# Kernel optimization log

Hardware: AMD Instinct MI355X
Metric: run time of the kernel (lower is better)

Reference implementation:

```python
import jax, jax.numpy as jnp
import numpy as np

B = 8          # graphs (FOVs)
NPG = 16384    # clusters per graph
N = B * NPG
K = 6          # knn k=5+1, loop=True
E = N * K
C0PG = 2048    # superclusters_0 per graph
C0 = B * C0PG
C1PG = 256     # superclusters_1 per graph
C1 = B * C1PG
L = 10         # 4 cluster-level + 3 SC0 + 3 SC1 PointTransformerConv layers
D = 64


def setup_inputs() -> dict:
    key = jax.random.key(0)
    ks = jax.random.split(key, 20)
    s = 0.05  # weight scale for stable attention logits
    x = jax.random.normal(ks[0], (N, D), jnp.float32)
    pos_c = jax.random.uniform(ks[1], (N, 2), jnp.float32)
    dst_c = jnp.repeat(jnp.arange(N, dtype=jnp.int32), K)
    src_c = jax.random.randint(ks[2], (E,), 0, N, jnp.int32)
    src_c = src_c.at[::K].set(jnp.arange(N, dtype=jnp.int32))  # self-loops
    batch = (jnp.arange(N, dtype=jnp.int32) // NPG)
    sc_id0 = (jnp.arange(N, dtype=jnp.int32) % C0PG)   # every SC0 id present per graph
    pos_sc0 = jax.random.uniform(ks[3], (C0, 2), jnp.float32)
    sc_id1 = (jnp.arange(C0, dtype=jnp.int32) % C1PG)
    pos_sc1 = jax.random.uniform(ks[4], (C1, 2), jnp.float32)
    return dict(
        x=x, pos_c=pos_c, src_c=src_c, dst_c=dst_c, batch=batch,
        sc_id0=sc_id0, pos_sc0=pos_sc0, sc_id1=sc_id1, pos_sc1=pos_sc1,
        Wlin=jax.random.normal(ks[5], (L, D, D)) * s,
        Wsrc=jax.random.normal(ks[6], (L, D, D)) * s,
        Wdst=jax.random.normal(ks[7], (L, D, D)) * s,
        pW1=jax.random.normal(ks[8], (L, 2, D)) * s,
        pB1=jnp.zeros((L, D), jnp.float32),
        pW2=jax.random.normal(ks[9], (L, D, D)) * s,
        pB2=jnp.zeros((L, D), jnp.float32),
        aW1=jax.random.normal(ks[10], (L, D, D)) * s,
        aB1=jnp.zeros((L, D), jnp.float32),
        aW2=jax.random.normal(ks[11], (L, D, D)) * s,
        aB2=jnp.zeros((L, D), jnp.float32),
        head_w=jax.random.normal(ks[12], (D, 2)) * s,
        head_b=jnp.zeros((2,), jnp.float32),
    )


def mlp2(x, W1, b1, W2, b2):
    # PyG MLP(plain_last=False): Linear->ReLU twice (eval mode, BN at init = identity)
    h = jax.nn.relu(x @ W1 + b1)
    return jax.nn.relu(h @ W2 + b2)


def ptconv(h, pos, src, dst, n, p, l):
    # PointTransformerConv: delta = pos_nn(pos_i - pos_j);
    # alpha = softmax_i(attn_nn(lin_dst(x)_i - lin_src(x)_j + delta));
    # out_i = max_j alpha * (lin(x)_j + delta)
    xv = h @ p['Wlin'][l]
    a_src = h @ p['Wsrc'][l]
    a_dst = h @ p['Wdst'][l]
    delta = mlp2(pos[dst] - pos[src], p['pW1'][l], p['pB1'][l], p['pW2'][l], p['pB2'][l])
    a = mlp2(a_dst[dst] - a_src[src] + delta, p['aW1'][l], p['aB1'][l], p['aW2'][l], p['aB2'][l])
    m = jax.ops.segment_max(a, dst, num_segments=n)
    e = jnp.exp(a - m[dst])
    ssum = jax.ops.segment_sum(e, dst, num_segments=n)
    alpha = e / ssum[dst]
    return jax.ops.segment_max(alpha * (xv[src] + delta), dst, num_segments=n)


def gen_cluster(ids, batch, nb):
    mx = jax.ops.segment_max(ids, batch, num_segments=nb)
    off = jnp.cumsum(jnp.concatenate([jnp.zeros((1,), ids.dtype), mx + 1]))
    return ids + off[batch].astype(ids.dtype)


def knn_edges(pos, b, npg, k):
    # knn_graph(k, loop=True) per graph: src=neighbor, dst=center
    p = pos.reshape(b, npg, 2)
    sq = jnp.sum(p * p, axis=-1)
    d2 = sq[:, :, None] + sq[:, None, :] - 2.0 * jnp.einsum('bnd,bmd->bnm', p, p)
    idx = jax.lax.top_k(-d2, k)[1]  # [b, npg, k], includes self (d=0)
    src = (idx + (jnp.arange(b) * npg)[:, None, None]).reshape(-1).astype(jnp.int32)
    dst = jnp.repeat(jnp.arange(b * npg, dtype=jnp.int32), k)
    return src, dst


def reference(x, pos_c, src_c, dst_c, batch, sc_id0, pos_sc0, sc_id1, pos_sc1,
              Wlin, Wsrc, Wdst, pW1, pB1, pW2, pB2, aW1, aB1, aW2, aB2,
              head_w, head_b):
    p = dict(Wlin=Wlin, Wsrc=Wsrc, Wdst=Wdst, pW1=pW1, pB1=pB1, pW2=pW2, pB2=pB2,
             aW1=aW1, aB1=aB1, aW2=aW2, aB2=aB2)
    h = x
    for l in range(4):  # cluster_encoder_0..3 on clusters graph
        h = ptconv(h, pos_c, src_c, dst_c, N, p, l)
    # pool clusters -> superclusters_0
    cl0 = gen_cluster(sc_id0, batch, B)
    h0 = jax.ops.segment_max(h, cl0, num_segments=C0)
    batch0 = jax.ops.segment_max(batch, cl0, num_segments=C0)
    src0, dst0 = knn_edges(pos_sc0, B, C0PG, K)
    for l in range(4, 7):
        h0 = ptconv(h0, pos_sc0, src0, dst0, C0, p, l)
    # pool SC0 -> superclusters_1
    cl1 = gen_cluster(sc_id1, batch0, B)
    h1 = jax.ops.segment_max(h0, cl1, num_segments=C1)
    batch1 = jax.ops.segment_max(batch0, cl1, num_segments=C1)
    src1, dst1 = knn_edges(pos_sc1, B, C1PG, K)
    for l in range(7, 10):
        h1 = ptconv(h1, pos_sc1, src1, dst1, C1, p, l)
    g = jax.ops.segment_max(h1, batch1, num_segments=B)  # global_max_pool
    return g @ head_w + head_b
```

## Files before the change

### kernel.cpp

```cpp
#include <hip/hip_runtime.h>
#include <cstdint>

namespace {
constexpr int BG   = 8;
constexpr int NPG  = 16384;
constexpr int NN   = BG * NPG;
constexpr int KK   = 6;
constexpr int C0PG = 2048;
constexpr int C0N  = BG * C0PG;
constexpr int C1PG = 256;
constexpr int C1N  = BG * C1PG;
constexpr int D    = 64;
constexpr int SEG0 = C0PG / 256;
constexpr int VS8  = 260;
constexpr int NMS  = 132;
}

__device__ __forceinline__ unsigned f2u_ord(float v) {
  unsigned u = __float_as_uint(v);
  return (u & 0x80000000u) ? ~u : (u | 0x80000000u);
}

__global__ void k_init_u32(unsigned* __restrict__ p, unsigned v, int n) {
  int i = blockIdx.x * blockDim.x + threadIdx.x;
  if (i < n) p[i] = v;
}

__global__ void k_seg_max_i32(const int* __restrict__ vals, const int* __restrict__ seg,
                              int* __restrict__ out, int n) {
  int i = blockIdx.x * blockDim.x + threadIdx.x;
  if (i < n) atomicMax(&out[seg[i]], vals[i]);
}

template <int NB>
__global__ __launch_bounds__(256) void k_seg_max_small(
    const int* __restrict__ vals, const int* __restrict__ seg,
    int* __restrict__ out, int n) {
  __shared__ int lmx[NB];
  int t = threadIdx.x;
  if (t < NB) lmx[t] = (int)0x80000000;
  __syncthreads();
  for (int i = blockIdx.x * 256 + t; i < n; i += gridDim.x * 256)
    atomicMax(&lmx[seg[i]], vals[i]);
  __syncthreads();
  if (t < NB) atomicMax(&out[t], lmx[t]);
}

__global__ void k_cumsum_off(const int* __restrict__ mx, int* __restrict__ off, int nb) {
  if (threadIdx.x == 0 && blockIdx.x == 0) {
    int a = 0; off[0] = 0;
    for (int b = 0; b < nb; ++b) { a += mx[b] + 1; off[b + 1] = a; }
  }
}

__global__ void k_gen_cl(const int* __restrict__ ids, const int* __restrict__ bt,
                         const int* __restrict__ off, int* __restrict__ cl, int n) {
  int i = blockIdx.x * blockDim.x + threadIdx.x;
  if (i < n) cl[i] = ids[i] + off[bt[i]];
}

__global__ void k_pool_f32(const float* __restrict__ h, const int* __restrict__ cl,
                           unsigned* __restrict__ outu, int total) {
  int i = blockIdx.x * blockDim.x + threadIdx.x;
  if (i < total) atomicMax(&outu[(size_t)cl[i >> 6] * D + (i & 63)], f2u_ord(h[i]));
}

__global__ void k_decode_f32(unsigned* __restrict__ p, int n) {
  int i = blockIdx.x * blockDim.x + threadIdx.x;
  if (i < n) { unsigned u = p[i]; p[i] = (u & 0x80000000u) ? (u ^ 0x80000000u) : ~u; }
}

__global__ __launch_bounds__(256) void k_knn(const float* __restrict__ pos, int npg,
                                             int* __restrict__ srcOut) {
  #pragma clang fp contract(off)
  __shared__ float px[2048], py[2048], sq[2048];
  int t = threadIdx.x;
  int nglob = blockIdx.x * 256 + t;
  int graph = nglob / npg;
  int base = graph * npg;
  for (int i = t; i < npg; i += 256) {
    float xx = pos[2 * (base + i)];
    float yy = pos[2 * (base + i) + 1];
    px[i] = xx; py[i] = yy;
    float a = xx * xx; float b = yy * yy;
    sq[i] = a + b;
  }
  __syncthreads();
  int i = nglob - base;
  float xi = px[i], yi = py[i], sqi = sq[i];
  float bd[KK]; int bi[KK];
  #pragma unroll
  for (int q = 0; q < KK; ++q) { bd[q] = 3.4e38f; bi[q] = 0; }
  for (int j = 0; j < npg; ++j) {
    float t1 = xi * px[j];
    float t2 = yi * py[j];
    float dot = t1 + t2;
    float d2 = (sqi + sq[j]) - 2.0f * dot;
    if (d2 < bd[KK - 1]) {
      bd[KK - 1] = d2; bi[KK - 1] = j;
      #pragma unroll
      for (int q = KK - 1; q > 0; --q) {
        if (bd[q] < bd[q - 1]) {
          float td = bd[q]; bd[q] = bd[q - 1]; bd[q - 1] = td;
          int ti = bi[q]; bi[q] = bi[q - 1]; bi[q - 1] = ti;
        }
      }
    }
  }
  #pragma unroll
  for (int q = 0; q < KK; ++q) srcOut[(size_t)nglob * KK + q] = base + bi[q];
}

__global__ __launch_bounds__(256) void k_knn_part(const float* __restrict__ pos, int npg,
                                                  int nseg,
                                                  float* __restrict__ outD,
                                                  int* __restrict__ outI) {
  #pragma clang fp contract(off)
  __shared__ float cx[256], cy[256], cs[256];
  int t = threadIdx.x;
  int qt = blockIdx.x / nseg;
  int s  = blockIdx.x % nseg;
  int qlo = qt * 256;
  int graph = qlo / npg;
  int base = graph * npg;
  int cbase = base + s * 256;
  {
    float xx = pos[2 * (cbase + t)];
    float yy = pos[2 * (cbase + t) + 1];
    cx[t] = xx; cy[t] = yy;
    float a = xx * xx; float b = yy * yy;
    cs[t] = a + b;
  }
  __syncthreads();
  int q = qlo + t;
  float xi = pos[2 * q], yi = pos[2 * q + 1];
  float qa = xi * xi; float qb = yi * yi;
  float sqi = qa + qb;
  float bd[KK]; int bi[KK];
  #pragma unroll
  for (int u = 0; u < KK; ++u) { bd[u] = 3.4e38f; bi[u] = 0; }
  for (int j = 0; j < 256; ++j) {
    float t1 = xi * cx[j];
    float t2 = yi * cy[j];
    float dot = t1 + t2;
    float d2 = (sqi + cs[j]) - 2.0f * dot;
    if (d2 < bd[KK - 1]) {
      bd[KK - 1] = d2; bi[KK - 1] = cbase + j;
      #pragma unroll
      for (int u = KK - 1; u > 0; --u) {
        if (bd[u] < bd[u - 1]) {
          float td = bd[u]; bd[u] = bd[u - 1]; bd[u - 1] = td;
          int ti = bi[u]; bi[u] = bi[u - 1]; bi[u - 1] = ti;
        }
      }
    }
  }
  size_t ob = (size_t)q * (nseg * KK) + (size_t)s * KK;
  #pragma unroll
  for (int u = 0; u < KK; ++u) { outD[ob + u] = bd[u]; outI[ob + u] = bi[u]; }
}

__global__ void k_knn_merge(const float* __restrict__ inD, const int* __restrict__ inI,
                            int nseg, int* __restrict__ srcOut, int nq) {
  int q = blockIdx.x * blockDim.x + threadIdx.x;
  if (q >= nq) return;
  float bd[KK]; int bi[KK];
  #pragma unroll
  for (int u = 0; u < KK; ++u) { bd[u] = 3.4e38f; bi[u] = 0x7fffffff; }
  size_t ib = (size_t)q * (nseg * KK);
  for (int e = 0; e < nseg * KK; ++e) {
    float d = inD[ib + e]; int ix = inI[ib + e];
    bool lt = (d < bd[KK - 1]) || (d == bd[KK - 1] && ix < bi[KK - 1]);
    if (lt) {
      bd[KK - 1] = d; bi[KK - 1] = ix;
      #pragma unroll
      for (int u = KK - 1; u > 0; --u) {
        bool sw = (bd[u] < bd[u - 1]) || (bd[u] == bd[u - 1] && bi[u] < bi[u - 1]);
        if (sw) {
          float td = bd[u]; bd[u] = bd[u - 1]; bd[u - 1] = td;
          int ti = bi[u]; bi[u] = bi[u - 1]; bi[u - 1] = ti;
        }
      }
    }
  }
  #pragma unroll
  for (int u = 0; u < KK; ++u) srcOut[(size_t)q * KK + u] = bi[u];
}

__global__ void __launch_bounds__(256)
__attribute__((amdgpu_waves_per_eu(4, 4)))
k_node_mm(const float* __restrict__ hin,
    const float* __restrict__ Wl, const float* __restrict__ Ws, const float* __restrict__ Wd,
    float* __restrict__ xv, float* __restrict__ as_, float* __restrict__ ad_) {
  __shared__ float wbuf[2048];
  __shared__ float vbuf[32 * NMS];
  int t = threadIdx.x;
  size_t nb = (size_t)blockIdx.x * 128;
  int ng = t >> 3, cb = t & 7, c0 = cb * 8;
  const float* Wm[3] = {Wl, Ws, Wd};
  float* Om[3] = {xv, as_, ad_};
  const float4* h4 = (const float4*)hin;
  float acc[3][32];
  #pragma unroll
  for (int m = 0; m < 3; ++m)
    #pragma unroll
    for (int i = 0; i < 32; ++i) acc[m][i] = 0.0f;
  for (int kh = 0; kh < 2; ++kh) {
    #pragma unroll
    for (int r = 0; r < 4; ++r) {
      int flat = r * 256 + t;
      int n = flat >> 3, kq = flat & 7;
      float4 hv = h4[(nb + n) * 16 + kh * 8 + kq];
      vbuf[(kq * 4 + 0) * NMS + n] = hv.x;
      vbuf[(kq * 4 + 1) * NMS + n] = hv.y;
      vbuf[(kq * 4 + 2) * NMS + n] = hv.z;
      vbuf[(kq * 4 + 3) * NMS + n] = hv.w;
    }
    #pragma unroll
    for (int m = 0; m < 3; ++m) {
      {
        const float4* w4 = (const float4*)Wm[m] + kh * 512;
        float4* wb = (float4*)wbuf;
        wb[t] = w4[t];
        wb[256 + t] = w4[256 + t];
      }
      __syncthreads();
      #pragma clang loop unroll_count(2)
      for (int kk = 0; kk < 32; ++kk) {
        float4 v4 = *(const float4*)&vbuf[kk * NMS + 4 * ng];
        float4 w0 = *(const float4*)&wbuf[kk * 64 + c0];
        float4 w1 = *(const float4*)&wbuf[kk * 64 + c0 + 4];
        float vv[4] = {v4.x, v4.y, v4.z, v4.w};
        float wv[8] = {w0.x, w0.y, w0.z, w0.w, w1.x, w1.y, w1.z, w1.w};
        #pragma unroll
        for (int ni = 0; ni < 4; ++ni)
          #pragma unroll
          for (int c = 0; c < 8; ++c)
            acc[m][ni * 8 + c] = fmaf(vv[ni], wv[c], acc[m][ni * 8 + c]);
      }
      __syncthreads();
    }
  }
  #pragma unroll
  for (int m = 0; m < 3; ++m) {
    float* O = Om[m];
    #pragma unroll
    for (int ni = 0; ni < 4; ++ni) {
      *(float4*)(O + (nb + 4 * ng + ni) * 64 + c0) =
          make_float4(acc[m][ni * 8 + 0], acc[m][ni * 8 + 1],
                      acc[m][ni * 8 + 2], acc[m][ni * 8 + 3]);
      *(float4*)(O + (nb + 4 * ng + ni) * 64 + c0 + 4) =
          make_float4(acc[m][ni * 8 + 4], acc[m][ni * 8 + 5],
                      acc[m][ni * 8 + 6], acc[m][ni * 8 + 7]);
    }
  }
}

__global__ void __launch_bounds__(256)
__attribute__((amdgpu_waves_per_eu(3, 3)))
k_edge_fused(
    const float* __restrict__ pos, const int* __restrict__ srcA,
    const float* __restrict__ as_, const float* __restrict__ ad_,
    const float* __restrict__ xv,
    const float* __restrict__ pW1, const float* __restrict__ pB1,
    const float* __restrict__ pW2, const float* __restrict__ pB2,
    const float* __restrict__ aW1, const float* __restrict__ aB1,
    const float* __restrict__ aW2, const float* __restrict__ aB2,
    float* __restrict__ hout) {
  __shared__ float wbuf[2048];
  __shared__ float vbuf[32 * VS8];
  __shared__ float sbuf[192];
  __shared__ float pdxs[192], pdys[192];
  __shared__ int   srcb[192];
  int t = threadIdx.x;
  int nb = blockIdx.x * 32;
  int ng = t >> 3;
  int cb = t & 7;
  int cl = 4 * cb;
  int ch = 32 + 4 * cb;
  int node = nb + ng;
  int ecol = 8 * ng;

  float4 wreg0 = ((const float4*)pW2)[t];
  float4 wreg1 = ((const float4*)pW2)[256 + t];
  int mycol = 8 * (t / 6) + (t % 6);
  if (t < 192) {
    int s = srcA[(size_t)nb * KK + t];
    srcb[t] = s;
    int dn = nb + t / KK;
    float2 pd = *(const float2*)(pos + 2 * (size_t)dn);
    float2 ps = *(const float2*)(pos + 2 * (size_t)s);
    pdxs[t] = pd.x - ps.x;
    pdys[t] = pd.y - ps.y;
    sbuf[t] = (t < 128) ? pW1[t] : pB1[t - 128];
  }
  __syncthreads();

  float d[48];
  {
    float4 b0 = *(const float4*)(pB2 + cl);
    float4 b1 = *(const float4*)(pB2 + ch);
    #pragma unroll
    for (int j = 0; j < 6; ++j) {
      d[j * 8 + 0] = b0.x; d[j * 8 + 1] = b0.y; d[j * 8 + 2] = b0.z; d[j * 8 + 3] = b0.w;
      d[j * 8 + 4] = b1.x; d[j * 8 + 5] = b1.y; d[j * 8 + 6] = b1.z; d[j * 8 + 7] = b1.w;
    }
  }
  #pragma unroll
  for (int h = 0; h < 2; ++h) {
    {
      float4* wb = (float4*)wbuf;
      wb[t] = wreg0;
      wb[256 + t] = wreg1;
    }
    {
      const float4* nxt = (h == 0) ? ((const float4*)pW2 + 512) : ((const float4*)aW1);
      wreg0 = nxt[t];
      wreg1 = nxt[256 + t];
    }
    if (t < 192) {
      float px = pdxs[t], py = pdys[t];
      #pragma clang loop unroll_count(4)
      for (int kk = 0; kk < 32; ++kk) {
        int k = h * 32 + kk;
        float p0 = px * sbuf[k];
        float p1 = py * sbuf[64 + k];
        float ph = fmaxf((p0 + p1) + sbuf[128 + k], 0.0f);
        vbuf[kk * VS8 + mycol] = ph;
      }
    }
    __syncthreads();
    #pragma clang loop unroll_count(2)
    for (int kk = 0; kk < 32; ++kk) {
      float4 va = *(const float4*)&vbuf[kk * VS8 + ecol];
      float4 vb = *(const float4*)&vbuf[kk * VS8 + ecol + 4];
      float4 w0 = *(const float4*)&wbuf[kk * 64 + cl];
      float4 w1 = *(const float4*)&wbuf[kk * 64 + ch];
      float vv[6] = {va.x, va.y, va.z, va.w, vb.x, vb.y};
      float wv[8] = {w0.x, w0.y, w0.z, w0.w, w1.x, w1.y, w1.z, w1.w};
      #pragma unroll
      for (int j = 0; j < 6; ++j)
        #pragma unroll
        for (int c = 0; c < 8; ++c)
          d[j * 8 + c] = fmaf(vv[j], wv[c], d[j * 8 + c]);
    }
    __syncthreads();
  }
  #pragma unroll
  for (int i = 0; i < 48; ++i) d[i] = fmaxf(d[i], 0.0f);

  float r[48];
  {
    float4 b0 = *(const float4*)(aB1 + cl);
    float4 b1 = *(const float4*)(aB1 + ch);
    #pragma unroll
    for (int j = 0; j < 6; ++j) {
      r[j * 8 + 0] = b0.x; r[j * 8 + 1] = b0.y; r[j * 8 + 2] = b0.z; r[j * 8 + 3] = b0.w;
      r[j * 8 + 4] = b1.x; r[j * 8 + 5] = b1.y; r[j * 8 + 6] = b1.z; r[j * 8 + 7] = b1.w;
    }
  }
  #pragma unroll
  for (int h = 0; h < 2; ++h) {
    {
      float4* wb = (float4*)wbuf;
      wb[t] = wreg0;
      wb[256 + t] = wreg1;
    }
    {
      const float4* nxt = (h == 0) ? ((const float4*)aW1 + 512) : ((const float4*)aW2);
      wreg0 = nxt[t];
      wreg1 = nxt[256 + t];
    }
    {
      int cbase = h ? ch : cl;
      float4 av = *(const float4*)(ad_ + (size_t)node * 64 + cbase);
      float vtmp[6][4];
      #pragma unroll
      for (int j = 0; j < 6; ++j) {
        int s = srcb[6 * ng + j];
        float4 sv = *(const float4*)(as_ + (size_t)s * 64 + cbase);
        vtmp[j][0] = (av.x - sv.x) + d[j * 8 + 4 * h + 0];
        vtmp[j][1] = (av.y - sv.y) + d[j * 8 + 4 * h + 1];
        vtmp[j][2] = (av.z - sv.z) + d[j * 8 + 4 * h + 2];
        vtmp[j][3] = (av.w - sv.w) + d[j * 8 + 4 * h + 3];
      }
      #pragma unroll
      for (int cj = 0; cj < 4; ++cj) {
        int rr = 4 * cb + cj;
        *(float4*)&vbuf[rr * VS8 + ecol] =
            make_float4(vtmp[0][cj], vtmp[1][cj], vtmp[2][cj], vtmp[3][cj]);
        *(float2*)&vbuf[rr * VS8 + ecol + 4] = make_float2(vtmp[4][cj], vtmp[5][cj]);
      }
    }
    __syncthreads();
    #pragma clang loop unroll_count(2)
    for (int kk = 0; kk < 32; ++kk) {
      float4 va = *(const float4*)&vbuf[kk * VS8 + ecol];
      float4 vb = *(const float4*)&vbuf[kk * VS8 + ecol + 4];
      float4 w0 = *(const float4*)&wbuf[kk * 64 + cl];
      float4 w1 = *(const float4*)&wbuf[kk * 64 + ch];
      float vv[6] = {va.x, va.y, va.z, va.w, vb.x, vb.y};
      float wv[8] = {w0.x, w0.y, w0.z, w0.w, w1.x, w1.y, w1.z, w1.w};
      #pragma unroll
      for (int j = 0; j < 6; ++j)
        #pragma unroll
        for (int c = 0; c < 8; ++c)
          r[j * 8 + c] = fmaf(vv[j], wv[c], r[j * 8 + c]);
    }
    __syncthreads();
  }
  #pragma unroll
  for (int i = 0; i < 48; ++i) r[i] = fmaxf(r[i], 0.0f);

  float a[48];
  {
    float4 b0 = *(const float4*)(aB2 + cl);
    float4 b1 = *(const float4*)(aB2 + ch);
    #pragma unroll
    for (int j = 0; j < 6; ++j) {
      a[j * 8 + 0] = b0.x; a[j * 8 + 1] = b0.y; a[j * 8 + 2] = b0.z; a[j * 8 + 3] = b0.w;
      a[j * 8 + 4] = b1.x; a[j * 8 + 5] = b1.y; a[j * 8 + 6] = b1.z; a[j * 8 + 7] = b1.w;
    }
  }
  #pragma unroll
  for (int h = 0; h < 2; ++h) {
    {
      float4* wb = (float4*)wbuf;
      wb[t] = wreg0;
      wb[256 + t] = wreg1;
    }
    if (h == 0) {
      const float4* nxt = (const float4*)aW2 + 512;
      wreg0 = nxt[t];
      wreg1 = nxt[256 + t];
    }
    #pragma unroll
    for (int cj = 0; cj < 4; ++cj) {
      int rr = 4 * cb + cj;
      *(float4*)&vbuf[rr * VS8 + ecol] =
          make_float4(r[0 * 8 + 4 * h + cj], r[1 * 8 + 4 * h + cj],
                      r[2 * 8 + 4 * h + cj], r[3 * 8 + 4 * h + cj]);
      *(float2*)&vbuf[rr * VS8 + ecol + 4] =
          make_float2(r[4 * 8 + 4 * h + cj], r[5 * 8 + 4 * h + cj]);
    }
    __syncthreads();
    #pragma clang loop unroll_count(2)
    for (int kk = 0; kk < 32; ++kk) {
      float4 va = *(const float4*)&vbuf[kk * VS8 + ecol];
      float4 vb = *(const float4*)&vbuf[kk * VS8 + ecol + 4];
      float4 w0 = *(const float4*)&wbuf[kk * 64 + cl];
      float4 w1 = *(const float4*)&wbuf[kk * 64 + ch];
      float vv[6] = {va.x, va.y, va.z, va.w, vb.x, vb.y};
      float wv[8] = {w0.x, w0.y, w0.z, w0.w, w1.x, w1.y, w1.z, w1.w};
      #pragma unroll
      for (int j = 0; j < 6; ++j)
        #pragma unroll
        for (int c = 0; c < 8; ++c)
          a[j * 8 + c] = fmaf(vv[j], wv[c], a[j * 8 + c]);
    }
    __syncthreads();
  }
  #pragma unroll
  for (int i = 0; i < 48; ++i) a[i] = fmaxf(a[i], 0.0f);

  float m8[8], ss[8], out[8];
  #pragma unroll
  for (int c = 0; c < 8; ++c) m8[c] = a[c];
  #pragma unroll
  for (int j = 1; j < 6; ++j)
    #pragma unroll
    for (int c = 0; c < 8; ++c) m8[c] = fmaxf(m8[c], a[j * 8 + c]);
  #pragma unroll
  for (int c = 0; c < 8; ++c) ss[c] = 0.0f;
  #pragma unroll
  for (int j = 0; j < 6; ++j)
    #pragma unroll
    for (int c = 0; c < 8; ++c) ss[c] += expf(a[j * 8 + c] - m8[c]);
  #pragma unroll
  for (int j = 0; j < 6; ++j) {
    int s = srcb[6 * ng + j];
    float4 x0 = *(const float4*)(xv + (size_t)s * 64 + cl);
    float4 x1 = *(const float4*)(xv + (size_t)s * 64 + ch);
    float xa[8] = {x0.x, x0.y, x0.z, x0.w, x1.x, x1.y, x1.z, x1.w};
    #pragma unroll
    for (int c = 0; c < 8; ++c) {
      float ej = expf(a[j * 8 + c] - m8[c]);
      float alpha = ej / ss[c];
      float val = alpha * (xa[c] + d[j * 8 + c]);
      out[c] = (j == 0) ? val : fmaxf(out[c], val);
    }
  }
  *(float4*)(hout + (size_t)node * 64 + cl) = make_float4(out[0], out[1], out[2], out[3]);
  *(float4*)(hout + (size_t)node * 64 + ch) = make_float4(out[4], out[5], out[6], out[7]);
}

__global__ void k_head(const float* __restrict__ g, const float* __restrict__ hw,
                       const float* __restrict__ hb, float* __restrict__ out) {
  int t = threadIdx.x;
  if (t >= BG * 2) return;
  int b = t >> 1, o = t & 1;
  float acc = 0.0f;
  for (int k = 0; k < D; ++k) acc = fmaf(g[b * D + k], hw[k * 2 + o], acc);
  out[b * 2 + o] = acc + hb[o];
}

extern "C" void kernel_launch(void* const* d_in, const int* in_sizes, int n_in,
                              void* d_out, int out_size, void* d_ws, size_t ws_size,
                              hipStream_t stream) {
  (void)in_sizes; (void)n_in; (void)out_size; (void)ws_size;
  const float* x      = (const float*)d_in[0];
  const float* pos_c  = (const float*)d_in[1];
  const int*   src_c  = (const int*)d_in[2];
  const int*   batch  = (const int*)d_in[4];
  const int*   sc_id0 = (const int*)d_in[5];
  const float* pos_s0 = (const float*)d_in[6];
  const int*   sc_id1 = (const int*)d_in[7];
  const float* pos_s1 = (const float*)d_in[8];
  const float* Wlin = (const float*)d_in[9];
  const float* Wsrc = (const float*)d_in[10];
  const float* Wdst = (const float*)d_in[11];
  const float* pW1  = (const float*)d_in[12];
  const float* pB1  = (const float*)d_in[13];
  const float* pW2  = (const float*)d_in[14];
  const float* pB2  = (const float*)d_in[15];
  const float* aW1  = (const float*)d_in[16];
  const float* aB1  = (const float*)d_in[17];
  const float* aW2  = (const float*)d_in[18];
  const float* aB2  = (const float*)d_in[19];
  const float* hw   = (const float*)d_in[20];
  const float* hb   = (const float*)d_in[21];
  float* outp = (float*)d_out;

  char* ws = (char*)d_ws;
  size_t off = 0;
  auto alloc = [&](size_t bytes) -> void* {
    void* p = ws + off; off = (off + bytes + 255) & ~(size_t)255; return p;
  };
  float* h   = (float*)alloc((size_t)NN * D * 4);
  float* xv  = (float*)alloc((size_t)NN * D * 4);
  float* as_ = (float*)alloc((size_t)NN * D * 4);
  float* ad_ = (float*)alloc((size_t)NN * D * 4);
  float* h0  = (float*)alloc((size_t)C0N * D * 4);
  float* h1  = (float*)alloc((size_t)C1N * D * 4);
  float* g   = (float*)alloc((size_t)BG * D * 4);
  int* cl0   = (int*)alloc((size_t)NN * 4);
  int* cl1   = (int*)alloc((size_t)C0N * 4);
  int* b0    = (int*)alloc((size_t)C0N * 4);
  int* b1    = (int*)alloc((size_t)C1N * 4);
  int* src0  = (int*)alloc((size_t)C0N * KK * 4);
  int* src1  = (int*)alloc((size_t)C1N * KK * 4);
  float* kd  = (float*)alloc((size_t)C0N * SEG0 * KK * 4);
  int*   ki  = (int*)alloc((size_t)C0N * SEG0 * KK * 4);
  int* mx    = (int*)alloc(256);
  int* offb  = (int*)alloc(256);

  auto ptconv = [&](int n, const float* pos, const int* srcA,
                    const float* hin, float* hout, int l) {
    k_node_mm<<<n / 128, 256, 0, stream>>>(hin,
        Wlin + (size_t)l * 4096, Wsrc + (size_t)l * 4096, Wdst + (size_t)l * 4096,
        xv, as_, ad_);
    k_edge_fused<<<n / 32, 256, 0, stream>>>(pos, srcA, as_, ad_, xv,
        pW1 + (size_t)l * 128, pB1 + (size_t)l * 64,
        pW2 + (size_t)l * 4096, pB2 + (size_t)l * 64,
        aW1 + (size_t)l * 4096, aB1 + (size_t)l * 64,
        aW2 + (size_t)l * 4096, aB2 + (size_t)l * 64,
        hout);
  };

  k_init_u32<<<1, 64, 0, stream>>>((unsigned*)mx, 0x80000000u, BG);
  k_seg_max_small<BG><<<64, 256, 0, stream>>>(sc_id0, batch, mx, NN);
  k_cumsum_off<<<1, 1, 0, stream>>>(mx, offb, BG);
  k_gen_cl<<<NN / 256, 256, 0, stream>>>(sc_id0, batch, offb, cl0, NN);
  k_init_u32<<<(C0N + 255) / 256, 256, 0, stream>>>((unsigned*)b0, 0x80000000u, C0N);
  k_seg_max_i32<<<NN / 256, 256, 0, stream>>>(batch, cl0, b0, NN);
  k_knn_part<<<(C0N / 256) * SEG0, 256, 0, stream>>>(pos_s0, C0PG, SEG0, kd, ki);
  k_knn_merge<<<C0N / 256, 256, 0, stream>>>(kd, ki, SEG0, src0, C0N);
  k_init_u32<<<1, 64, 0, stream>>>((unsigned*)mx, 0x80000000u, BG);
  k_seg_max_small<BG><<<64, 256, 0, stream>>>(sc_id1, b0, mx, C0N);
  k_cumsum_off<<<1, 1, 0, stream>>>(mx, offb, BG);
  k_gen_cl<<<C0N / 256, 256, 0, stream>>>(sc_id1, b0, offb, cl1, C0N);
  k_init_u32<<<(C1N + 255) / 256, 256, 0, stream>>>((unsigned*)b1, 0x80000000u, C1N);
  k_seg_max_i32<<<C0N / 256, 256, 0, stream>>>(b0, cl1, b1, C0N);
  k_knn<<<C1N / 256, 256, 0, stream>>>(pos_s1, C1PG, src1);

  ptconv(NN, pos_c, src_c, x, h, 0);
  for (int l = 1; l < 4; ++l) ptconv(NN, pos_c, src_c, h, h, l);
  k_init_u32<<<C0N * D / 256, 256, 0, stream>>>((unsigned*)h0, 0x007fffffu, C0N * D);
  k_pool_f32<<<NN * D / 256, 256, 0, stream>>>(h, cl0, (unsigned*)h0, NN * D);
  k_decode_f32<<<C0N * D / 256, 256, 0, stream>>>((unsigned*)h0, C0N * D);
  for (int l = 4; l < 7; ++l) ptconv(C0N, pos_s0, src0, h0, h0, l);
  k_init_u32<<<C1N * D / 256, 256, 0, stream>>>((unsigned*)h1, 0x007fffffu, C1N * D);
  k_pool_f32<<<C0N * D / 256, 256, 0, stream>>>(h0, cl1, (unsigned*)h1, C0N * D);
  k_decode_f32<<<C1N * D / 256, 256, 0, stream>>>((unsigned*)h1, C1N * D);
  for (int l = 7; l < 10; ++l) ptconv(C1N, pos_s1, src1, h1, h1, l);
  k_init_u32<<<(BG * D + 255) / 256, 256, 0, stream>>>((unsigned*)g, 0x007fffffu, BG * D);
  k_pool_f32<<<C1N * D / 256, 256, 0, stream>>>(h1, b1, (unsigned*)g, C1N * D);
  k_decode_f32<<<(BG * D + 255) / 256, 256, 0, stream>>>((unsigned*)g, BG * D);
  k_head<<<1, 64, 0, stream>>>(g, hw, hb, outp);
}
```

Before: 1.874 ms.

## Read weights directly from global/L1 instead of LDS staging; skew vbuf rows

Removes the shared-memory weight buffer in the node and edge matmul kernels. Weights are now read straight from global memory, which is cached and uniform across node groups, so the per-stage copy into shared memory and its register prefetch go away. The edge kernel also rotates vbuf row indices by node group to spread shared-memory bank accesses. The trade-off is more vector-memory load instructions inside the inner FMA loops, which can stall on cache latency, while lowering LDS use and register pressure.

Measured after the change: 2.467 ms. +31.6%, slower.

```diff
diff --git a/kernel.cpp b/kernel.cpp
--- a/kernel.cpp
+++ b/kernel.cpp
@@ -192,7 +192,6 @@
 k_node_mm(const float* __restrict__ hin,
     const float* __restrict__ Wl, const float* __restrict__ Ws, const float* __restrict__ Wd,
     float* __restrict__ xv, float* __restrict__ as_, float* __restrict__ ad_) {
-  __shared__ float wbuf[2048];
   __shared__ float vbuf[32 * NMS];
   int t = threadIdx.x;
   size_t nb = (size_t)blockIdx.x * 128;
@@ -206,6 +205,7 @@
     #pragma unroll
     for (int i = 0; i < 32; ++i) acc[m][i] = 0.0f;
   for (int kh = 0; kh < 2; ++kh) {
+    if (kh) __syncthreads();
     #pragma unroll
     for (int r = 0; r < 4; ++r) {
       int flat = r * 256 + t;
@@ -216,20 +216,15 @@
       vbuf[(kq * 4 + 2) * NMS + n] = hv.z;
       vbuf[(kq * 4 + 3) * NMS + n] = hv.w;
     }
+    __syncthreads();
     #pragma unroll
     for (int m = 0; m < 3; ++m) {
-      {
-        const float4* w4 = (const float4*)Wm[m] + kh * 512;
-        float4* wb = (float4*)wbuf;
-        wb[t] = w4[t];
-        wb[256 + t] = w4[256 + t];
-      }
-      __syncthreads();
+      const float4* Wg = (const float4*)(Wm[m] + (size_t)kh * 2048);
       #pragma clang loop unroll_count(2)
       for (int kk = 0; kk < 32; ++kk) {
         float4 v4 = *(const float4*)&vbuf[kk * NMS + 4 * ng];
-        float4 w0 = *(const float4*)&wbuf[kk * 64 + c0];
-        float4 w1 = *(const float4*)&wbuf[kk * 64 + c0 + 4];
+        float4 w0 = Wg[kk * 16 + 2 * cb];
+        float4 w1 = Wg[kk * 16 + 2 * cb + 1];
         float vv[4] = {v4.x, v4.y, v4.z, v4.w};
         float wv[8] = {w0.x, w0.y, w0.z, w0.w, w1.x, w1.y, w1.z, w1.w};
         #pragma unroll
@@ -238,7 +233,6 @@
           for (int c = 0; c < 8; ++c)
             acc[m][ni * 8 + c] = fmaf(vv[ni], wv[c], acc[m][ni * 8 + c]);
       }
-      __syncthreads();
     }
   }
   #pragma unroll
@@ -267,7 +261,6 @@
     const float* __restrict__ aW1, const float* __restrict__ aB1,
     const float* __restrict__ aW2, const float* __restrict__ aB2,
     float* __restrict__ hout) {
-  __shared__ float wbuf[2048];
   __shared__ float vbuf[32 * VS8];
   __shared__ float sbuf[192];
   __shared__ float pdxs[192], pdys[192];
@@ -281,14 +274,12 @@
   int node = nb + ng;
   int ecol = 8 * ng;
 
-  float4 wreg0 = ((const float4*)pW2)[t];
-  float4 wreg1 = ((const float4*)pW2)[256 + t];
-  int mycol = 8 * (t / 6) + (t % 6);
+  int nd = t / 6;
+  int mycol = 8 * nd + (t % 6);
   if (t < 192) {
     int s = srcA[(size_t)nb * KK + t];
     srcb[t] = s;
-    int dn = nb + t / KK;
-    float2 pd = *(const float2*)(pos + 2 * (size_t)dn);
+    float2 pd = *(const float2*)(pos + 2 * (size_t)(nb + nd));
     float2 ps = *(const float2*)(pos + 2 * (size_t)s);
     pdxs[t] = pd.x - ps.x;
     pdys[t] = pd.y - ps.y;
@@ -308,16 +299,6 @@
   }
   #pragma unroll
   for (int h = 0; h < 2; ++h) {
-    {
-      float4* wb = (float4*)wbuf;
-      wb[t] = wreg0;
-      wb[256 + t] = wreg1;
-    }
-    {
-      const float4* nxt = (h == 0) ? ((const float4*)pW2 + 512) : ((const float4*)aW1);
-      wreg0 = nxt[t];
-      wreg1 = nxt[256 + t];
-    }
     if (t < 192) {
       float px = pdxs[t], py = pdys[t];
       #pragma clang loop unroll_count(4)
@@ -326,23 +307,27 @@
         float p0 = px * sbuf[k];
         float p1 = py * sbuf[64 + k];
         float ph = fmaxf((p0 + p1) + sbuf[128 + k], 0.0f);
-        vbuf[kk * VS8 + mycol] = ph;
-      }
-    }
-    __syncthreads();
-    #pragma clang loop unroll_count(2)
-    for (int kk = 0; kk < 32; ++kk) {
-      float4 va = *(const float4*)&vbuf[kk * VS8 + ecol];
-      float4 vb = *(const float4*)&vbuf[kk * VS8 + ecol + 4];
-      float4 w0 = *(const float4*)&wbuf[kk * 64 + cl];
-      float4 w1 = *(const float4*)&wbuf[kk * 64 + ch];
-      float vv[6] = {va.x, va.y, va.z, va.w, vb.x, vb.y};
-      float wv[8] = {w0.x, w0.y, w0.z, w0.w, w1.x, w1.y, w1.z, w1.w};
-      #pragma unroll
-      for (int j = 0; j < 6; ++j)
+        vbuf[((kk + nd) & 31) * VS8 + mycol] = ph;
+      }
+    }
+    __syncthreads();
+    {
+      const float4* Wg = (const float4*)(pW2 + (size_t)h * 2048);
+      #pragma clang loop unroll_count(2)
+      for (int kk = 0; kk < 32; ++kk) {
+        int rrow = (kk + ng) & 31;
+        float4 va = *(const float4*)&vbuf[rrow * VS8 + ecol];
+        float4 vb = *(const float4*)&vbuf[rrow * VS8 + ecol + 4];
+        float4 w0 = Wg[kk * 16 + cb];
+        float4 w1 = Wg[kk * 16 + 8 + cb];
+        float vv[6] = {va.x, va.y, va.z, va.w, vb.x, vb.y};
+        float wv[8] = {w0.x, w0.y, w0.z, w0.w, w1.x, w1.y, w1.z, w1.w};
         #pragma unroll
-        for (int c = 0; c < 8; ++c)
-          d[j * 8 + c] = fmaf(vv[j], wv[c], d[j * 8 + c]);
+        for (int j = 0; j < 6; ++j)
+          #pragma unroll
+          for (int c = 0; c < 8; ++c)
+            d[j * 8 + c] = fmaf(vv[j], wv[c], d[j * 8 + c]);
+      }
     }
     __syncthreads();
   }
@@ -361,16 +346,6 @@
   }
   #pragma unroll
   for (int h = 0; h < 2; ++h) {
-    {
-      float4* wb = (float4*)wbuf;
-      wb[t] = wreg0;
-      wb[256 + t] = wreg1;
-    }
-    {
-      const float4* nxt = (h == 0) ? ((const float4*)aW1 + 512) : ((const float4*)aW2);
-      wreg0 = nxt[t];
-      wreg1 = nxt[256 + t];
-    }
     {
       int cbase = h ? ch : cl;
       float4 av = *(const float4*)(ad_ + (size_t)node * 64 + cbase);
@@ -386,26 +361,30 @@
       }
       #pragma unroll
       for (int cj = 0; cj < 4; ++cj) {
-        int rr = 4 * cb + cj;
-        *(float4*)&vbuf[rr * VS8 + ecol] =
+        int prow = (4 * cb + cj + ng) & 31;
+        *(float4*)&vbuf[prow * VS8 + ecol] =
             make_float4(vtmp[0][cj], vtmp[1][cj], vtmp[2][cj], vtmp[3][cj]);
-        *(float2*)&vbuf[rr * VS8 + ecol + 4] = make_float2(vtmp[4][cj], vtmp[5][cj]);
-      }
-    }
-    __syncthreads();
-    #pragma clang loop unroll_count(2)
-    for (int kk = 0; kk < 32; ++kk) {
-      float4 va = *(const float4*)&vbuf[kk * VS8 + ecol];
-      float4 vb = *(const float4*)&vbuf[kk * VS8 + ecol + 4];
-      float4 w0 = *(const float4*)&wbuf[kk * 64 + cl];
-      float4 w1 = *(const float4*)&wbuf[kk * 64 + ch];
-      float vv[6] = {va.x, va.y, va.z, va.w, vb.x, vb.y};
-      float wv[8] = {w0.x, w0.y, w0.z, w0.w, w1.x, w1.y, w1.z, w1.w};
-      #pragma unroll
-      for (int j = 0; j < 6; ++j)
+        *(float2*)&vbuf[prow * VS8 + ecol + 4] = make_float2(vtmp[4][cj], vtmp[5][cj]);
+      }
+    }
+    __syncthreads();
+    {
+      const float4* Wg = (const float4*)(aW1 + (size_t)h * 2048);
+      #pragma clang loop unroll_count(2)
+      for (int kk = 0; kk < 32; ++kk) {
+        int rrow = (kk + ng) & 31;
+        float4 va = *(const float4*)&vbuf[rrow * VS8 + ecol];
+        float4 vb = *(const float4*)&vbuf[rrow * VS8 + ecol + 4];
+        float4 w0 = Wg[kk * 16 + cb];
+        float4 w1 = Wg[kk * 16 + 8 + cb];
+        float vv[6] = {va.x, va.y, va.z, va.w, vb.x, vb.y};
+        float wv[8] = {w0.x, w0.y, w0.z, w0.w, w1.x, w1.y, w1.z, w1.w};
         #pragma unroll
-        for (int c = 0; c < 8; ++c)
-          r[j * 8 + c] = fmaf(vv[j], wv[c], r[j * 8 + c]);
+        for (int j = 0; j < 6; ++j)
+          #pragma unroll
+          for (int c = 0; c < 8; ++c)
+            r[j * 8 + c] = fmaf(vv[j], wv[c], r[j * 8 + c]);
+      }
     }
     __syncthreads();
   }
@@ -424,39 +403,33 @@
   }
   #pragma unroll
   for (int h = 0; h < 2; ++h) {
-    {
-      float4* wb = (float4*)wbuf;
-      wb[t] = wreg0;
-      wb[256 + t] = wreg1;
-    }
-    if (h == 0) {
-      const float4* nxt = (const float4*)aW2 + 512;
-      wreg0 = nxt[t];
-      wreg1 = nxt[256 + t];
-    }
     #pragma unroll
     for (int cj = 0; cj < 4; ++cj) {
-      int rr = 4 * cb + cj;
-      *(float4*)&vbuf[rr * VS8 + ecol] =
+      int prow = (4 * cb + cj + ng) & 31;
+      *(float4*)&vbuf[prow * VS8 + ecol] =
           make_float4(r[0 * 8 + 4 * h + cj], r[1 * 8 + 4 * h + cj],
                       r[2 * 8 + 4 * h + cj], r[3 * 8 + 4 * h + cj]);
-      *(float2*)&vbuf[rr * VS8 + ecol + 4] =
+      *(float2*)&vbuf[prow * VS8 + ecol + 4] =
           make_float2(r[4 * 8 + 4 * h + cj], r[5 * 8 + 4 * h + cj]);
     }
     __syncthreads();
-    #pragma clang loop unroll_count(2)
-    for (int kk = 0; kk < 32; ++kk) {
-      float4 va = *(const float4*)&vbuf[kk * VS8 + ecol];
-      float4 vb = *(const float4*)&vbuf[kk * VS8 + ecol + 4];
-      float4 w0 = *(const float4*)&wbuf[kk * 64 + cl];
-      float4 w1 = *(const float4*)&wbuf[kk * 64 + ch];
-      float vv[6] = {va.x, va.y, va.z, va.w, vb.x, vb.y};
-      float wv[8] = {w0.x, w0.y, w0.z, w0.w, w1.x, w1.y, w1.z, w1.w};
-      #pragma unroll
-      for (int j = 0; j < 6; ++j)
+    {
+      const float4* Wg = (const float4*)(aW2 + (size_t)h * 2048);
+      #pragma clang loop unroll_count(2)
+      for (int kk = 0; kk < 32; ++kk) {
+        int rrow = (kk + ng) & 31;
+        float4 va = *(const float4*)&vbuf[rrow * VS8 + ecol];
+        float4 vb = *(const float4*)&vbuf[rrow * VS8 + ecol + 4];
+        float4 w0 = Wg[kk * 16 + cb];
+        float4 w1 = Wg[kk * 16 + 8 + cb];
+        float vv[6] = {va.x, va.y, va.z, va.w, vb.x, vb.y};
+        float wv[8] = {w0.x, w0.y, w0.z, w0.w, w1.x, w1.y, w1.z, w1.w};
         #pragma unroll
-        for (int c = 0; c < 8; ++c)
-          a[j * 8 + c] = fmaf(vv[j], wv[c], a[j * 8 + c]);
+        for (int j = 0; j < 6; ++j)
+          #pragma unroll
+          for (int c = 0; c < 8; ++c)
+            a[j * 8 + c] = fmaf(vv[j], wv[c], a[j * 8 + c]);
+      }
     }
     __syncthreads();
   }
```
